# Kernel optimization log

Measured on AMD Instinct MI355X. Metric: run time of the kernel, lower is better.

The kernel has to match this reference:

```python
import jax, jax.numpy as jnp
import numpy as np

DIM = 1024
D_STATE = 16
D_CONV = 4
EXPAND = 2
D_INNER = EXPAND * DIM          # 2048
DT_RANK = DIM // 16             # 64 (mamba default: ceil(d_model/16))
BATCH = 2
SEQ = 2048


def setup_inputs() -> dict:
    key = jax.random.key(0)
    ks = jax.random.split(key, 32)
    s = 0.02
    def mk(k, shape):
        return jax.random.normal(k, shape, jnp.float32) * s
    inp = {}
    inp["hidden_state"] = jax.random.normal(ks[0], (BATCH, SEQ, DIM), jnp.float32)
    inp["mask"] = jax.random.bernoulli(ks[1], 0.7, (BATCH, SEQ)).astype(jnp.float32)
    inp["mask_proj_w"] = mk(ks[2], (DIM, 1))
    inp["mask_proj_b"] = mk(ks[3], (DIM,))
    i = 4
    A_init = jnp.log(jnp.broadcast_to(jnp.arange(1, D_STATE + 1, dtype=jnp.float32), (D_INNER, D_STATE)))
    for p in ("f", "b"):
        inp[p + "_in_w"]   = mk(ks[i], (2 * D_INNER, DIM)); i += 1
        inp[p + "_conv_w"] = mk(ks[i], (D_INNER, D_CONV)); i += 1
        inp[p + "_conv_b"] = mk(ks[i], (D_INNER,)); i += 1
        inp[p + "_xproj_w"] = mk(ks[i], (DT_RANK + 2 * D_STATE, D_INNER)); i += 1
        inp[p + "_dt_w"]   = mk(ks[i], (D_INNER, DT_RANK)); i += 1
        inp[p + "_dt_b"]   = mk(ks[i], (D_INNER,)) + 1.0  # softplus(~1) -> moderate dt
        i += 1
        inp[p + "_A_log"]  = A_init
        inp[p + "_D"]      = jnp.ones((D_INNER,), jnp.float32)
        inp[p + "_out_w"]  = mk(ks[i], (DIM, D_INNER)); i += 1
    return inp


def _mamba(x, in_w, conv_w, conv_b, xproj_w, dt_w, dt_b, A_log, Dp, out_w):
    # x: [B, L, DIM]
    Bsz = x.shape[0]
    xz = x @ in_w.T                                  # [B, L, 2*D_INNER]
    xi, z = jnp.split(xz, 2, axis=-1)
    # causal depthwise conv1d over time
    xc = jnp.transpose(xi, (0, 2, 1))                # [B, D_INNER, L]
    xc = jax.lax.conv_general_dilated(
        xc, conv_w[:, None, :], window_strides=(1,),
        padding=[(D_CONV - 1, 0)], feature_group_count=D_INNER)
    xc = xc + conv_b[None, :, None]
    u = jax.nn.silu(jnp.transpose(xc, (0, 2, 1)))    # [B, L, D_INNER]
    dbc = u @ xproj_w.T                              # [B, L, DT_RANK + 2*D_STATE]
    dt, Bm, Cm = jnp.split(dbc, [DT_RANK, DT_RANK + D_STATE], axis=-1)
    delta = jax.nn.softplus(dt @ dt_w.T + dt_b)      # [B, L, D_INNER]
    A = -jnp.exp(A_log)                              # [D_INNER, D_STATE]
    dA = jnp.exp(jnp.einsum('bld,dn->bldn', delta, A))
    dBu = jnp.einsum('bld,bln,bld->bldn', delta, Bm, u)
    def step(h, inps):
        dA_t, dBu_t, C_t = inps                      # [B,D_INNER,D_STATE], [B,D_INNER,D_STATE], [B,D_STATE]
        h = dA_t * h + dBu_t
        y = jnp.einsum('bdn,bn->bd', h, C_t)
        return h, y
    h0 = jnp.zeros((Bsz, D_INNER, D_STATE), x.dtype)
    xs = (jnp.moveaxis(dA, 1, 0), jnp.moveaxis(dBu, 1, 0), jnp.moveaxis(Cm, 1, 0))
    _, ys = jax.lax.scan(step, h0, xs)               # ys: [L, B, D_INNER]
    y = jnp.moveaxis(ys, 0, 1) + u * Dp              # [B, L, D_INNER]
    y = y * jax.nn.silu(z)
    return y @ out_w.T                               # [B, L, DIM]


def reference(hidden_state, mask, mask_proj_w, mask_proj_b,
              f_in_w, f_conv_w, f_conv_b, f_xproj_w, f_dt_w, f_dt_b, f_A_log, f_D, f_out_w,
              b_in_w, b_conv_w, b_conv_b, b_xproj_w, b_dt_w, b_dt_b, b_A_log, b_D, b_out_w):
    m = mask[..., None]                              # [B, L, 1]
    mask_features = m @ mask_proj_w.T + mask_proj_b  # [B, L, DIM]
    x_masked = hidden_state * m + mask_features * (1.0 - m)
    forward_out = _mamba(x_masked, f_in_w, f_conv_w, f_conv_b, f_xproj_w,
                         f_dt_w, f_dt_b, f_A_log, f_D, f_out_w)
    backward_out = jnp.flip(
        _mamba(jnp.flip(x_masked, 1), b_in_w, b_conv_w, b_conv_b, b_xproj_w,
               b_dt_w, b_dt_b, b_A_log, b_D, b_out_w), 1)
    ssm_output = forward_out + backward_out
    return ssm_output * m + hidden_state * (1.0 - m)
```

## Files before the change

### kernel.cpp

```cpp
#include <hip/hip_runtime.h>
#include <hip/hip_bf16.h>
#include <stdint.h>

typedef unsigned short u16;
using bf16x8 = __attribute__((ext_vector_type(8))) short;
using f32x4  = __attribute__((ext_vector_type(4))) float;
typedef unsigned short u16x4 __attribute__((ext_vector_type(4)));

#define AS1 __attribute__((address_space(1)))
#define AS3 __attribute__((address_space(3)))

__device__ __forceinline__ float bf2f(u16 x) {
    union { unsigned int u; float f; } v; v.u = ((unsigned int)x) << 16; return v.f;
}
__device__ __forceinline__ u16 f2bf(float f) {
    union { float f; unsigned int u; } v; v.f = f;
    return (u16)((v.u + 0x7fffu + ((v.u >> 16) & 1u)) >> 16);
}

#define ACT_NONE 0
#define ACT_SOFTPLUS 1

__global__ __launch_bounds__(256) void gemm_bt_kernel(
    const u16* __restrict__ A, int lda,
    const u16* __restrict__ B,
    float* __restrict__ Cf, u16* __restrict__ Cb,
    const float* __restrict__ bias,
    int ldc, int M, int N, int K, int Nreal,
    int flipA, int flipC, int act)
{
    __shared__ __align__(16) u16 As[128 * 64];
    __shared__ __align__(16) u16 Bs[128 * 64];

    const int tid  = threadIdx.x;
    const int bm   = blockIdx.y * 128;
    const int bn   = blockIdx.x * 128;
    const int lane = tid & 63;
    const int wid  = tid >> 6;
    const int wr   = (wid >> 1) * 64;
    const int wc   = (wid & 1) * 64;
    const int l15  = lane & 15;
    const int l4   = lane >> 4;

    f32x4 acc[4][4];
    const f32x4 vzero = {0.f, 0.f, 0.f, 0.f};
    #pragma unroll
    for (int i = 0; i < 4; ++i)
        #pragma unroll
        for (int j = 0; j < 4; ++j) acc[i][j] = vzero;

    const int nK = K >> 6;
    for (int k0 = 0; k0 < nK; ++k0) {
        #pragma unroll
        for (int i = 0; i < 4; ++i) {
            int off  = i * 4096 + tid * 16;
            int row  = off >> 7;
            int colB = off & 127;
            int rowG = bm + row;
            if (flipA) { int b = rowG >> 11; int l = rowG & 2047; rowG = (b << 11) + (2047 - l); }
            const char* src = (const char*)A + ((size_t)rowG * lda + ((size_t)k0 << 6)) * 2 + colB;
            __builtin_amdgcn_global_load_lds((const AS1 unsigned int*)src,
                                             (AS3 unsigned int*)((char*)As + off), 16, 0, 0);
        }
        #pragma unroll
        for (int i = 0; i < 4; ++i) {
            int off  = i * 4096 + tid * 16;
            int row  = off >> 7;
            int colB = off & 127;
            int rowG = bn + row;
            const char* src = (const char*)B + ((size_t)rowG * K + ((size_t)k0 << 6)) * 2 + colB;
            __builtin_amdgcn_global_load_lds((const AS1 unsigned int*)src,
                                             (AS3 unsigned int*)((char*)Bs + off), 16, 0, 0);
        }
        __syncthreads();

        #pragma unroll
        for (int kk = 0; kk < 2; ++kk) {
            bf16x8 af[4], bfr[4];
            #pragma unroll
            for (int mt = 0; mt < 4; ++mt) {
                int row = wr + mt * 16 + l15;
                af[mt] = *(const bf16x8*)((const char*)As + row * 128 + kk * 64 + l4 * 16);
            }
            #pragma unroll
            for (int nt = 0; nt < 4; ++nt) {
                int row = wc + nt * 16 + l15;
                bfr[nt] = *(const bf16x8*)((const char*)Bs + row * 128 + kk * 64 + l4 * 16);
            }
            #pragma unroll
            for (int mt = 0; mt < 4; ++mt)
                #pragma unroll
                for (int nt = 0; nt < 4; ++nt)
                    acc[mt][nt] = __builtin_amdgcn_mfma_f32_16x16x32_bf16(
                        af[mt], bfr[nt], acc[mt][nt], 0, 0, 0);
        }
        __syncthreads();
    }

    #pragma unroll
    for (int mt = 0; mt < 4; ++mt) {
        #pragma unroll
        for (int nt = 0; nt < 4; ++nt) {
            int col = bn + wc + nt * 16 + l15;
            if (col >= Nreal) continue;
            #pragma unroll
            for (int r = 0; r < 4; ++r) {
                int rowG = bm + wr + mt * 16 + l4 * 4 + r;
                float v = acc[mt][nt][r];
                if (act == ACT_SOFTPLUS) {
                    v += bias[col];
                    v = fmaxf(v, 0.f) + log1pf(__expf(-fabsf(v)));
                }
                int rw = rowG;
                if (flipC) { int b = rw >> 11; int l = rw & 2047; rw = (b << 11) + (2047 - l); }
                if (Cb) Cb[(size_t)rw * ldc + col] = f2bf(v);
                else    Cf[(size_t)rw * ldc + col] = v;
            }
        }
    }
}

__global__ void conv_silu_kernel(const u16* __restrict__ xz,
                                 const float* __restrict__ cw,
                                 const float* __restrict__ cb,
                                 u16* __restrict__ u)
{
    int d  = blockIdx.x * 256 + threadIdx.x;
    int r0 = blockIdx.y * 16;
    float w0 = cw[d*4+0], w1 = cw[d*4+1], w2 = cw[d*4+2], w3 = cw[d*4+3];
    float bias = cb[d];
    float x1, x2, x3;
    if (r0 & 2047) {
        x1 = bf2f(xz[(size_t)(r0-1) * 4096 + d]);
        x2 = bf2f(xz[(size_t)(r0-2) * 4096 + d]);
        x3 = bf2f(xz[(size_t)(r0-3) * 4096 + d]);
    } else { x1 = x2 = x3 = 0.f; }
    #pragma unroll
    for (int i = 0; i < 16; ++i) {
        int r = r0 + i;
        float x0 = bf2f(xz[(size_t)r * 4096 + d]);
        float acc = fmaf(w3, x0, fmaf(w2, x1, fmaf(w1, x2, fmaf(w0, x3, bias))));
        float sig = 1.f / (1.f + __expf(-acc));
        u[(size_t)r * 2048 + d] = f2bf(acc * sig);
        x3 = x2; x2 = x1; x1 = x0;
    }
}


#define NCH 32
#define CSZ 64
#define SUB 16
#define LW  264

__global__ __launch_bounds__(256) void scan_part1(
    const u16* __restrict__ delta, const u16* __restrict__ u,
    const float* __restrict__ dbc, const float* __restrict__ A_log,
    float* __restrict__ P, float* __restrict__ S)
{
    __shared__ __align__(16) u16   dl_s[SUB * LW];
    __shared__ __align__(16) u16   ul_s[SUB * LW];
    __shared__ __align__(16) float b_s[SUB * 16];

    const int tid = threadIdx.x;
    const int d0  = blockIdx.x * 256;
    const int c   = blockIdx.y;
    const int b   = blockIdx.z;
    const int d   = d0 + tid;
    const size_t rbase = (size_t)b * 2048 + c * CSZ;

    float a2[16], h[16], p[16];
    #pragma unroll
    for (int q = 0; q < 4; ++q) {
        float4 al = *(const float4*)&A_log[(size_t)d * 16 + q * 4];
        a2[q*4+0] = -__expf(al.x) * 1.4426950408889634f;
        a2[q*4+1] = -__expf(al.y) * 1.4426950408889634f;
        a2[q*4+2] = -__expf(al.z) * 1.4426950408889634f;
        a2[q*4+3] = -__expf(al.w) * 1.4426950408889634f;
    }
    #pragma unroll
    for (int n = 0; n < 16; ++n) { h[n] = 0.f; p[n] = 1.f; }

    const int sr  = tid >> 4;
    const int sc16 = (tid & 15) * 16;

    for (int sch = 0; sch < CSZ / SUB; ++sch) {
        {
            size_t row = rbase + sch * SUB + sr;
            *(bf16x8*)&dl_s[sr * LW + sc16]     = *(const bf16x8*)&delta[row * 2048 + d0 + sc16];
            *(bf16x8*)&dl_s[sr * LW + sc16 + 8] = *(const bf16x8*)&delta[row * 2048 + d0 + sc16 + 8];
            *(bf16x8*)&ul_s[sr * LW + sc16]     = *(const bf16x8*)&u[row * 2048 + d0 + sc16];
            *(bf16x8*)&ul_s[sr * LW + sc16 + 8] = *(const bf16x8*)&u[row * 2048 + d0 + sc16 + 8];
            if (tid < 64) {
                int r2 = tid >> 2, c4 = (tid & 3) * 4;
                size_t g2 = rbase + sch * SUB + r2;
                *(float4*)&b_s[r2 * 16 + c4] = *(const float4*)&dbc[g2 * 96 + 64 + c4];
            }
        }
        __syncthreads();
        for (int s = 0; s < SUB; ++s) {
            float dv  = bf2f(dl_s[s * LW + tid]);
            float uv  = bf2f(ul_s[s * LW + tid]);
            float dvu = dv * uv;
            const float4* Bp = (const float4*)&b_s[s * 16];
            #pragma unroll
            for (int q = 0; q < 4; ++q) {
                float4 Bq = Bp[q];
                #pragma unroll
                for (int j = 0; j < 4; ++j) {
                    int n = q * 4 + j;
                    float dA = exp2f(dv * a2[n]);
                    h[n] = fmaf(dA, h[n], dvu * ((&Bq.x)[j]));
                    p[n] *= dA;
                }
            }
        }
        __syncthreads();
    }

    size_t base = (((size_t)(b * NCH + c)) << 15) + (size_t)d * 16;
    #pragma unroll
    for (int q = 0; q < 4; ++q) {
        float4 pv = { p[q*4+0], p[q*4+1], p[q*4+2], p[q*4+3] };
        float4 sv = { h[q*4+0], h[q*4+1], h[q*4+2], h[q*4+3] };
        *(float4*)&P[base + q * 4] = pv;
        *(float4*)&S[base + q * 4] = sv;
    }
}

__global__ void scan_part2(const float* __restrict__ P, float* __restrict__ S)
{
    int i  = blockIdx.x * 256 + threadIdx.x;
    int b  = i >> 15;
    int dn = i & 32767;
    size_t base = ((size_t)b * NCH) << 15;
    float h = 0.f;
    #pragma unroll 4
    for (int c = 0; c < NCH; ++c) {
        size_t idx = base + ((size_t)c << 15) + dn;
        float p = P[idx];
        float s = S[idx];
        S[idx] = h;
        h = fmaf(p, h, s);
    }
}

__global__ __launch_bounds__(256) void scan_part3(
    const u16* __restrict__ delta, const u16* __restrict__ u,
    const float* __restrict__ dbc, const u16* __restrict__ xz,
    const float* __restrict__ A_log, const float* __restrict__ Dp,
    const float* __restrict__ Hin, u16* __restrict__ y)
{
    __shared__ __align__(16) u16   dl_s[SUB * LW];
    __shared__ __align__(16) u16   ul_s[SUB * LW];
    __shared__ __align__(16) u16   zl_s[SUB * LW];
    __shared__ __align__(16) float bc_s[SUB * 32];

    const int tid = threadIdx.x;
    const int d0  = blockIdx.x * 256;
    const int c   = blockIdx.y;
    const int b   = blockIdx.z;
    const int d   = d0 + tid;
    const size_t rbase = (size_t)b * 2048 + c * CSZ;

    float a2[16], h[16];
    #pragma unroll
    for (int q = 0; q < 4; ++q) {
        float4 al = *(const float4*)&A_log[(size_t)d * 16 + q * 4];
        a2[q*4+0] = -__expf(al.x) * 1.4426950408889634f;
        a2[q*4+1] = -__expf(al.y) * 1.4426950408889634f;
        a2[q*4+2] = -__expf(al.z) * 1.4426950408889634f;
        a2[q*4+3] = -__expf(al.w) * 1.4426950408889634f;
    }
    {
        size_t base = (((size_t)(b * NCH + c)) << 15) + (size_t)d * 16;
        #pragma unroll
        for (int q = 0; q < 4; ++q) {
            float4 hv = *(const float4*)&Hin[base + q * 4];
            h[q*4+0] = hv.x; h[q*4+1] = hv.y; h[q*4+2] = hv.z; h[q*4+3] = hv.w;
        }
    }
    const float Dd = Dp[d];

    const int sr   = tid >> 4;
    const int sc16 = (tid & 15) * 16;

    for (int sch = 0; sch < CSZ / SUB; ++sch) {
        {
            size_t row = rbase + sch * SUB + sr;
            *(bf16x8*)&dl_s[sr * LW + sc16]     = *(const bf16x8*)&delta[row * 2048 + d0 + sc16];
            *(bf16x8*)&dl_s[sr * LW + sc16 + 8] = *(const bf16x8*)&delta[row * 2048 + d0 + sc16 + 8];
            *(bf16x8*)&ul_s[sr * LW + sc16]     = *(const bf16x8*)&u[row * 2048 + d0 + sc16];
            *(bf16x8*)&ul_s[sr * LW + sc16 + 8] = *(const bf16x8*)&u[row * 2048 + d0 + sc16 + 8];
            *(bf16x8*)&zl_s[sr * LW + sc16]     = *(const bf16x8*)&xz[row * 4096 + 2048 + d0 + sc16];
            *(bf16x8*)&zl_s[sr * LW + sc16 + 8] = *(const bf16x8*)&xz[row * 4096 + 2048 + d0 + sc16 + 8];
            if (tid < 128) {
                int r2 = tid >> 3, c4 = (tid & 7) * 4;
                size_t g2 = rbase + sch * SUB + r2;
                *(float4*)&bc_s[r2 * 32 + c4] = *(const float4*)&dbc[g2 * 96 + 64 + c4];
            }
        }
        __syncthreads();
        for (int s = 0; s < SUB; ++s) {
            float dv  = bf2f(dl_s[s * LW + tid]);
            float uv  = bf2f(ul_s[s * LW + tid]);
            float dvu = dv * uv;
            float yv  = 0.f;
            const float4* Bp = (const float4*)&bc_s[s * 32];
            const float4* Cp = (const float4*)&bc_s[s * 32 + 16];
            #pragma unroll
            for (int q = 0; q < 4; ++q) {
                float4 Bq = Bp[q];
                float4 Cq = Cp[q];
                #pragma unroll
                for (int j = 0; j < 4; ++j) {
                    int n = q * 4 + j;
                    float dA = exp2f(dv * a2[n]);
                    h[n] = fmaf(dA, h[n], dvu * ((&Bq.x)[j]));
                    yv   = fmaf(h[n], ((&Cq.x)[j]), yv);
                }
            }
            float zv  = bf2f(zl_s[s * LW + tid]);
            float sig = 1.f / (1.f + __expf(-zv));
            float out = (yv + uv * Dd) * (zv * sig);
            y[(rbase + sch * SUB + s) * 2048 + d] = f2bf(out);
        }
        __syncthreads();
    }
}

__global__ void blend_kernel(const float* __restrict__ hidden, const float* __restrict__ mask,
                             const float* __restrict__ mw, const float* __restrict__ mb,
                             u16* __restrict__ xm)
{
    size_t i = (size_t)blockIdx.x * 256 + threadIdx.x;
    int r = (int)(i >> 10), c = (int)(i & 1023);
    float m = mask[r];
    float v = hidden[i] * m + (m * mw[c] + mb[c]) * (1.f - m);
    xm[i] = f2bf(v);
}

__global__ void final_kernel(const float* __restrict__ hidden, const float* __restrict__ mask,
                             const float* __restrict__ fo, const float* __restrict__ bo,
                             float* __restrict__ out)
{
    size_t i = (size_t)blockIdx.x * 256 + threadIdx.x;
    int r = (int)(i >> 10);
    float m = mask[r];
    out[i] = (fo[i] + bo[i]) * m + hidden[i] * (1.f - m);
}

__global__ void cvt_kernel(const float* __restrict__ src, u16* __restrict__ dst, int n) {
    int i = blockIdx.x * 256 + threadIdx.x;
    if (i < n) dst[i] = f2bf(src[i]);
}
__global__ void cvt_pad_kernel(const float* __restrict__ src, u16* __restrict__ dst,
                               int rows_src, int cols, int n_dst) {
    int i = blockIdx.x * 256 + threadIdx.x;
    if (i >= n_dst) return;
    int r = i / cols;
    dst[i] = (r < rows_src) ? f2bf(src[(size_t)r * cols + (i % cols)]) : (u16)0;
}
__global__ void cvt_dt_kernel(const float* __restrict__ dbc, u16* __restrict__ dst) {
    int i = blockIdx.x * 256 + threadIdx.x;
    int r = i >> 6, c = i & 63;
    dst[i] = f2bf(dbc[(size_t)r * 96 + c]);
}

extern "C" void kernel_launch(void* const* d_in, const int* in_sizes, int n_in,
                              void* d_out, int out_size, void* d_ws, size_t ws_size,
                              hipStream_t stream)
{
    (void)in_sizes; (void)n_in; (void)out_size; (void)ws_size;
    const float* hidden = (const float*)d_in[0];
    const float* mask   = (const float*)d_in[1];
    const float* mpw    = (const float*)d_in[2];
    const float* mpb    = (const float*)d_in[3];

    char* ws = (char*)d_ws;
    size_t off = 0;
    auto alloc = [&](size_t bytes) -> char* {
        char* p = ws + off; off += (bytes + 255) & ~(size_t)255; return p;
    };
    u16*   xm    = (u16*)  alloc(4096ull * 1024 * 2);
    u16*   xz    = (u16*)  alloc(4096ull * 4096 * 2);
    u16*   ub    = (u16*)  alloc(4096ull * 2048 * 2);
    float* dbc   = (float*)alloc(4096ull * 96 * 4);
    u16*   dtb   = (u16*)  alloc(4096ull * 64 * 2);
    u16*   delta = (u16*)  alloc(4096ull * 2048 * 2);
    u16*   yb    = (u16*)  alloc(4096ull * 2048 * 2);
    float* fout  = (float*)alloc(4096ull * 1024 * 4);
    float* bout  = (float*)alloc(4096ull * 1024 * 4);
    float* Pbuf  = (float*)alloc(2ull * NCH * 2048 * 16 * 4);
    float* Sbuf  = (float*)alloc(2ull * NCH * 2048 * 16 * 4);
    u16* w_in[2]  = { (u16*)alloc(4096ull*1024*2), (u16*)alloc(4096ull*1024*2) };
    u16* w_xp[2]  = { (u16*)alloc(128ull*2048*2),  (u16*)alloc(128ull*2048*2)  };
    u16* w_dt[2]  = { (u16*)alloc(2048ull*64*2),   (u16*)alloc(2048ull*64*2)   };
    u16* w_out[2] = { (u16*)alloc(1024ull*2048*2), (u16*)alloc(1024ull*2048*2) };

    for (int dir = 0; dir < 2; ++dir) {
        int base = 4 + dir * 9;
        cvt_kernel<<<(4096*1024)/256, 256, 0, stream>>>((const float*)d_in[base+0], w_in[dir], 4096*1024);
        cvt_pad_kernel<<<(128*2048)/256, 256, 0, stream>>>((const float*)d_in[base+3], w_xp[dir], 96, 2048, 128*2048);
        cvt_kernel<<<(2048*64)/256, 256, 0, stream>>>((const float*)d_in[base+4], w_dt[dir], 2048*64);
        cvt_kernel<<<(1024*2048)/256, 256, 0, stream>>>((const float*)d_in[base+8], w_out[dir], 1024*2048);
    }
    blend_kernel<<<16384, 256, 0, stream>>>(hidden, mask, mpw, mpb, xm);

    for (int dir = 0; dir < 2; ++dir) {
        int base = 4 + dir * 9;
        const float* conv_w = (const float*)d_in[base+1];
        const float* conv_b = (const float*)d_in[base+2];
        const float* dt_b   = (const float*)d_in[base+5];
        const float* A_log  = (const float*)d_in[base+6];
        const float* Dp     = (const float*)d_in[base+7];
        int flip = dir;

        gemm_bt_kernel<<<dim3(32, 32), 256, 0, stream>>>(
            xm, 1024, w_in[dir], nullptr, xz, nullptr, 4096, 4096, 4096, 1024, 4096, flip, 0, ACT_NONE);
        conv_silu_kernel<<<dim3(8, 256), 256, 0, stream>>>(xz, conv_w, conv_b, ub);
        gemm_bt_kernel<<<dim3(1, 32), 256, 0, stream>>>(
            ub, 2048, w_xp[dir], dbc, nullptr, nullptr, 96, 4096, 128, 2048, 96, 0, 0, ACT_NONE);
        cvt_dt_kernel<<<(4096*64)/256, 256, 0, stream>>>(dbc, dtb);
        gemm_bt_kernel<<<dim3(16, 32), 256, 0, stream>>>(
            dtb, 64, w_dt[dir], nullptr, delta, dt_b, 2048, 4096, 2048, 64, 2048, 0, 0, ACT_SOFTPLUS);
        scan_part1<<<dim3(8, NCH, 2), 256, 0, stream>>>(delta, ub, dbc, A_log, Pbuf, Sbuf);
        scan_part2<<<256, 256, 0, stream>>>(Pbuf, Sbuf);
        scan_part3<<<dim3(8, NCH, 2), 256, 0, stream>>>(delta, ub, dbc, xz, A_log, Dp, Sbuf, yb);
        gemm_bt_kernel<<<dim3(8, 32), 256, 0, stream>>>(
            yb, 2048, w_out[dir], dir ? bout : fout, nullptr, nullptr, 1024, 4096, 1024, 2048, 1024, 0, flip, ACT_NONE);
    }
    final_kernel<<<16384, 256, 0, stream>>>(hidden, mask, fout, bout, (float*)d_out);
}
```

Baseline: 813.2 us.

## Double-buffer GEMM tiles, split-K xproj, fuse final blend and weight conversion

The GEMM now double-buffers its LDS tiles so the next K tile's global-to-LDS loads are issued before the current tile's MFMAs run. The narrow x_proj GEMM is split along K into four slices that accumulate with atomics into a zeroed buffer, which raises parallelism for a launch that had only 32 blocks. The final mask blend is fused into the backward out-projection epilogue, removing a separate kernel and an intermediate buffer. The eight weight-conversion launches are merged into one. The trade-offs are twice the LDS per block, which can lower occupancy, atomic contention, and an extra memset.

New measurement: 816.2 us. About the same (+0.4%).

```diff
diff --git a/kernel.cpp b/kernel.cpp
--- a/kernel.cpp
+++ b/kernel.cpp
@@ -27,10 +27,12 @@
     float* __restrict__ Cf, u16* __restrict__ Cb,
     const float* __restrict__ bias,
     int ldc, int M, int N, int K, int Nreal,
-    int flipA, int flipC, int act)
-{
-    __shared__ __align__(16) u16 As[128 * 64];
-    __shared__ __align__(16) u16 Bs[128 * 64];
+    int flipA, int flipC, int act, int kSlices,
+    const float* __restrict__ addC, const float* __restrict__ hid,
+    const float* __restrict__ msk)
+{
+    __shared__ __align__(16) u16 As[2][128 * 64];
+    __shared__ __align__(16) u16 Bs[2][128 * 64];
 
     const int tid  = threadIdx.x;
     const int bm   = blockIdx.y * 128;
@@ -42,6 +44,10 @@
     const int l15  = lane & 15;
     const int l4   = lane >> 4;
 
+    const int kLen = K / kSlices;
+    const int kt0  = (blockIdx.z * kLen) >> 6;
+    const int nK   = kLen >> 6;
+
     f32x4 acc[4][4];
     const f32x4 vzero = {0.f, 0.f, 0.f, 0.f};
     #pragma unroll
@@ -49,8 +55,7 @@
         #pragma unroll
         for (int j = 0; j < 4; ++j) acc[i][j] = vzero;
 
-    const int nK = K >> 6;
-    for (int k0 = 0; k0 < nK; ++k0) {
+    auto stage = [&](int buf, int kt) {
         #pragma unroll
         for (int i = 0; i < 4; ++i) {
             int off  = i * 4096 + tid * 16;
@@ -58,9 +63,9 @@
             int colB = off & 127;
             int rowG = bm + row;
             if (flipA) { int b = rowG >> 11; int l = rowG & 2047; rowG = (b << 11) + (2047 - l); }
-            const char* src = (const char*)A + ((size_t)rowG * lda + ((size_t)k0 << 6)) * 2 + colB;
+            const char* src = (const char*)A + ((size_t)rowG * lda + ((size_t)kt << 6)) * 2 + colB;
             __builtin_amdgcn_global_load_lds((const AS1 unsigned int*)src,
-                                             (AS3 unsigned int*)((char*)As + off), 16, 0, 0);
+                                             (AS3 unsigned int*)((char*)As[buf] + off), 16, 0, 0);
         }
         #pragma unroll
         for (int i = 0; i < 4; ++i) {
@@ -68,11 +73,18 @@
             int row  = off >> 7;
             int colB = off & 127;
             int rowG = bn + row;
-            const char* src = (const char*)B + ((size_t)rowG * K + ((size_t)k0 << 6)) * 2 + colB;
+            const char* src = (const char*)B + ((size_t)rowG * K + ((size_t)kt << 6)) * 2 + colB;
             __builtin_amdgcn_global_load_lds((const AS1 unsigned int*)src,
-                                             (AS3 unsigned int*)((char*)Bs + off), 16, 0, 0);
-        }
-        __syncthreads();
+                                             (AS3 unsigned int*)((char*)Bs[buf] + off), 16, 0, 0);
+        }
+    };
+
+    stage(0, kt0);
+    __syncthreads();
+
+    int cur = 0;
+    for (int t = 0; t < nK; ++t) {
+        if (t + 1 < nK) stage(cur ^ 1, kt0 + t + 1);
 
         #pragma unroll
         for (int kk = 0; kk < 2; ++kk) {
@@ -80,12 +92,12 @@
             #pragma unroll
             for (int mt = 0; mt < 4; ++mt) {
                 int row = wr + mt * 16 + l15;
-                af[mt] = *(const bf16x8*)((const char*)As + row * 128 + kk * 64 + l4 * 16);
+                af[mt] = *(const bf16x8*)((const char*)As[cur] + row * 128 + kk * 64 + l4 * 16);
             }
             #pragma unroll
             for (int nt = 0; nt < 4; ++nt) {
                 int row = wc + nt * 16 + l15;
-                bfr[nt] = *(const bf16x8*)((const char*)Bs + row * 128 + kk * 64 + l4 * 16);
+                bfr[nt] = *(const bf16x8*)((const char*)Bs[cur] + row * 128 + kk * 64 + l4 * 16);
             }
             #pragma unroll
             for (int mt = 0; mt < 4; ++mt)
@@ -95,6 +107,7 @@
                         af[mt], bfr[nt], acc[mt][nt], 0, 0, 0);
         }
         __syncthreads();
+        cur ^= 1;
     }
 
     #pragma unroll
@@ -113,8 +126,18 @@
                 }
                 int rw = rowG;
                 if (flipC) { int b = rw >> 11; int l = rw & 2047; rw = (b << 11) + (2047 - l); }
-                if (Cb) Cb[(size_t)rw * ldc + col] = f2bf(v);
-                else    Cf[(size_t)rw * ldc + col] = v;
+                size_t ci = (size_t)rw * ldc + col;
+                if (kSlices > 1) {
+                    atomicAdd(&Cf[ci], v);
+                } else if (addC) {
+                    float m = msk[rw];
+                    float tot = v + addC[ci];
+                    Cf[ci] = tot * m + hid[ci] * (1.f - m);
+                } else if (Cb) {
+                    Cb[ci] = f2bf(v);
+                } else {
+                    Cf[ci] = v;
+                }
             }
         }
     }
@@ -145,7 +168,6 @@
         x3 = x2; x2 = x1; x1 = x0;
     }
 }
-
 
 #define NCH 32
 #define CSZ 64
@@ -339,27 +361,33 @@
     xm[i] = f2bf(v);
 }
 
-__global__ void final_kernel(const float* __restrict__ hidden, const float* __restrict__ mask,
-                             const float* __restrict__ fo, const float* __restrict__ bo,
-                             float* __restrict__ out)
+struct CvtArgs { const float* src[8]; u16* dst[8]; };
+__global__ void cvt_weights_kernel(CvtArgs a)
 {
     size_t i = (size_t)blockIdx.x * 256 + threadIdx.x;
-    int r = (int)(i >> 10);
-    float m = mask[r];
-    out[i] = (fo[i] + bo[i]) * m + hidden[i] * (1.f - m);
-}
-
-__global__ void cvt_kernel(const float* __restrict__ src, u16* __restrict__ dst, int n) {
-    int i = blockIdx.x * 256 + threadIdx.x;
-    if (i < n) dst[i] = f2bf(src[i]);
-}
-__global__ void cvt_pad_kernel(const float* __restrict__ src, u16* __restrict__ dst,
-                               int rows_src, int cols, int n_dst) {
-    int i = blockIdx.x * 256 + threadIdx.x;
-    if (i >= n_dst) return;
-    int r = i / cols;
-    dst[i] = (r < rows_src) ? f2bf(src[(size_t)r * cols + (i % cols)]) : (u16)0;
-}
+    if (i < 8388608) {
+        int s = (int)(i >> 22);
+        size_t j = i & 4194303;
+        a.dst[s][j] = f2bf(a.src[s][j]);
+    } else if (i < 12582912) {
+        size_t k = i - 8388608;
+        int s = 2 + (int)(k >> 21);
+        size_t j = k & 2097151;
+        a.dst[s][j] = f2bf(a.src[s][j]);
+    } else if (i < 12845056) {
+        size_t k = i - 12582912;
+        int s = 4 + (int)(k >> 17);
+        size_t j = k & 131071;
+        a.dst[s][j] = f2bf(a.src[s][j]);
+    } else if (i < 13369344) {
+        size_t k = i - 12845056;
+        int s = 6 + (int)(k >> 18);
+        size_t j = k & 262143;
+        int r = (int)(j >> 11), c = (int)(j & 2047);
+        a.dst[s][j] = (r < 96) ? f2bf(a.src[s][(size_t)r * 2048 + c]) : (u16)0;
+    }
+}
+
 __global__ void cvt_dt_kernel(const float* __restrict__ dbc, u16* __restrict__ dst) {
     int i = blockIdx.x * 256 + threadIdx.x;
     int r = i >> 6, c = i & 63;
@@ -389,7 +417,6 @@
     u16*   delta = (u16*)  alloc(4096ull * 2048 * 2);
     u16*   yb    = (u16*)  alloc(4096ull * 2048 * 2);
     float* fout  = (float*)alloc(4096ull * 1024 * 4);
-    float* bout  = (float*)alloc(4096ull * 1024 * 4);
     float* Pbuf  = (float*)alloc(2ull * NCH * 2048 * 16 * 4);
     float* Sbuf  = (float*)alloc(2ull * NCH * 2048 * 16 * 4);
     u16* w_in[2]  = { (u16*)alloc(4096ull*1024*2), (u16*)alloc(4096ull*1024*2) };
@@ -397,12 +424,17 @@
     u16* w_dt[2]  = { (u16*)alloc(2048ull*64*2),   (u16*)alloc(2048ull*64*2)   };
     u16* w_out[2] = { (u16*)alloc(1024ull*2048*2), (u16*)alloc(1024ull*2048*2) };
 
-    for (int dir = 0; dir < 2; ++dir) {
-        int base = 4 + dir * 9;
-        cvt_kernel<<<(4096*1024)/256, 256, 0, stream>>>((const float*)d_in[base+0], w_in[dir], 4096*1024);
-        cvt_pad_kernel<<<(128*2048)/256, 256, 0, stream>>>((const float*)d_in[base+3], w_xp[dir], 96, 2048, 128*2048);
-        cvt_kernel<<<(2048*64)/256, 256, 0, stream>>>((const float*)d_in[base+4], w_dt[dir], 2048*64);
-        cvt_kernel<<<(1024*2048)/256, 256, 0, stream>>>((const float*)d_in[base+8], w_out[dir], 1024*2048);
+    {
+        CvtArgs ca;
+        ca.src[0] = (const float*)d_in[4];  ca.dst[0] = w_in[0];
+        ca.src[1] = (const float*)d_in[13]; ca.dst[1] = w_in[1];
+        ca.src[2] = (const float*)d_in[12]; ca.dst[2] = w_out[0];
+        ca.src[3] = (const float*)d_in[21]; ca.dst[3] = w_out[1];
+        ca.src[4] = (const float*)d_in[8];  ca.dst[4] = w_dt[0];
+        ca.src[5] = (const float*)d_in[17]; ca.dst[5] = w_dt[1];
+        ca.src[6] = (const float*)d_in[7];  ca.dst[6] = w_xp[0];
+        ca.src[7] = (const float*)d_in[16]; ca.dst[7] = w_xp[1];
+        cvt_weights_kernel<<<(13369344 + 255) / 256, 256, 0, stream>>>(ca);
     }
     blend_kernel<<<16384, 256, 0, stream>>>(hidden, mask, mpw, mpb, xm);
 
@@ -415,19 +447,29 @@
         const float* Dp     = (const float*)d_in[base+7];
         int flip = dir;
 
-        gemm_bt_kernel<<<dim3(32, 32), 256, 0, stream>>>(
-            xm, 1024, w_in[dir], nullptr, xz, nullptr, 4096, 4096, 4096, 1024, 4096, flip, 0, ACT_NONE);
+        gemm_bt_kernel<<<dim3(32, 32, 1), 256, 0, stream>>>(
+            xm, 1024, w_in[dir], nullptr, xz, nullptr, 4096, 4096, 4096, 1024, 4096,
+            flip, 0, ACT_NONE, 1, nullptr, nullptr, nullptr);
         conv_silu_kernel<<<dim3(8, 256), 256, 0, stream>>>(xz, conv_w, conv_b, ub);
-        gemm_bt_kernel<<<dim3(1, 32), 256, 0, stream>>>(
-            ub, 2048, w_xp[dir], dbc, nullptr, nullptr, 96, 4096, 128, 2048, 96, 0, 0, ACT_NONE);
+        hipMemsetAsync(dbc, 0, 4096ull * 96 * 4, stream);
+        gemm_bt_kernel<<<dim3(1, 32, 4), 256, 0, stream>>>(
+            ub, 2048, w_xp[dir], dbc, nullptr, nullptr, 96, 4096, 128, 2048, 96,
+            0, 0, ACT_NONE, 4, nullptr, nullptr, nullptr);
         cvt_dt_kernel<<<(4096*64)/256, 256, 0, stream>>>(dbc, dtb);
-        gemm_bt_kernel<<<dim3(16, 32), 256, 0, stream>>>(
-            dtb, 64, w_dt[dir], nullptr, delta, dt_b, 2048, 4096, 2048, 64, 2048, 0, 0, ACT_SOFTPLUS);
+        gemm_bt_kernel<<<dim3(16, 32, 1), 256, 0, stream>>>(
+            dtb, 64, w_dt[dir], nullptr, delta, dt_b, 2048, 4096, 2048, 64, 2048,
+            0, 0, ACT_SOFTPLUS, 1, nullptr, nullptr, nullptr);
         scan_part1<<<dim3(8, NCH, 2), 256, 0, stream>>>(delta, ub, dbc, A_log, Pbuf, Sbuf);
         scan_part2<<<256, 256, 0, stream>>>(Pbuf, Sbuf);
         scan_part3<<<dim3(8, NCH, 2), 256, 0, stream>>>(delta, ub, dbc, xz, A_log, Dp, Sbuf, yb);
-        gemm_bt_kernel<<<dim3(8, 32), 256, 0, stream>>>(
-            yb, 2048, w_out[dir], dir ? bout : fout, nullptr, nullptr, 1024, 4096, 1024, 2048, 1024, 0, flip, ACT_NONE);
-    }
-    final_kernel<<<16384, 256, 0, stream>>>(hidden, mask, fout, bout, (float*)d_out);
-}
+        if (dir == 0) {
+            gemm_bt_kernel<<<dim3(8, 32, 1), 256, 0, stream>>>(
+                yb, 2048, w_out[0], fout, nullptr, nullptr, 1024, 4096, 1024, 2048, 1024,
+                0, 0, ACT_NONE, 1, nullptr, nullptr, nullptr);
+        } else {
+            gemm_bt_kernel<<<dim3(8, 32, 1), 256, 0, stream>>>(
+                yb, 2048, w_out[1], (float*)d_out, nullptr, nullptr, 1024, 4096, 1024, 2048, 1024,
+                0, 1, ACT_NONE, 1, fout, hidden, mask);
+        }
+    }
+}
```
